# Optimization experiments

Measured on AMD Instinct MI355X. Metric: run time of the kernel, lower is better.

The kernel has to match this reference:

```python
import jax, jax.numpy as jnp
import numpy as np
import math

B, S, D, H = 4, 2048, 2048, 16
HD = D // H  # 128


def _alibi_slopes(n_heads):
    # standard ALiBi slopes: 2^(-8/n * (h+1))
    return jnp.asarray([2.0 ** (-8.0 / n_heads * (h + 1)) for h in range(n_heads)], dtype=jnp.float32)


def setup_inputs() -> dict:
    key = jax.random.key(0)
    ks = jax.random.split(key, 10)
    w = lambda k: jax.random.normal(k, (D, D), dtype=jnp.float32) * 0.02
    b = lambda k: jax.random.normal(k, (D,), dtype=jnp.float32) * 0.01
    return {
        "hidden_states": jax.random.normal(ks[0], (B, S, D), dtype=jnp.float32),
        "Wq": w(ks[1]), "bq": b(ks[2]),
        "Wk": w(ks[3]), "bk": b(ks[4]),
        "Wv": w(ks[5]), "bv": b(ks[6]),
        "Wo": w(ks[7]), "bo": b(ks[8]),
        "alibi_slopes": _alibi_slopes(H),
    }


def reference(hidden_states, Wq, bq, Wk, bk, Wv, bv, Wo, bo, alibi_slopes):
    Bn, t, _ = hidden_states.shape
    split = lambda x: x.reshape(Bn, t, H, HD).transpose(0, 2, 1, 3)  # [B,H,S,hd]
    q = split(hidden_states @ Wq.T + bq)
    k = split(hidden_states @ Wk.T + bk)
    v = split(hidden_states @ Wv.T + bv)

    scores = jnp.einsum("bhsd,bhtd->bhst", q, k)  # [B,H,S,S]
    pos = jnp.arange(t)
    # alibi bias added BEFORE the 1/sqrt(hd) scaling, as in the torch code
    rel = (pos[None, :] - pos[:, None]).astype(scores.dtype)  # j - i
    bias = alibi_slopes[:, None, None] * rel  # [H,S,S]
    scores = (scores + bias[None]) / math.sqrt(HD)
    # grok-style tanh rescaling
    scores = 30.0 * jnp.tanh(scores / 30.0)
    causal = pos[:, None] >= pos[None, :]  # [S,S]
    scores = jnp.where(causal[None, None], scores, -jnp.inf)
    probs = jax.nn.softmax(scores, axis=-1)
    ctx = jnp.einsum("bhst,bhtd->bhsd", probs, v)
    ctx = ctx.transpose(0, 2, 1, 3).reshape(Bn, t, D)
    return ctx @ Wo.T + bo
```

## Files before the change

kernel.cpp:

```cpp
#include <hip/hip_runtime.h>

typedef unsigned int u32;
typedef unsigned short u16;
typedef __bf16 bf16x8 __attribute__((ext_vector_type(8)));
typedef float f32x4 __attribute__((ext_vector_type(4)));


__device__ __forceinline__ u16 f2bf(float f) {
  u32 u = __builtin_bit_cast(u32, f);
  u32 r = u + 0x7fffu + ((u >> 16) & 1u);
  return (u16)(r >> 16);
}

__device__ __forceinline__ void gload_lds16(const void* g, void* l) {
  __builtin_amdgcn_global_load_lds(
      (__attribute__((address_space(1))) void*)(g),
      (__attribute__((address_space(3))) void*)(l), 16, 0, 0);
}


__global__ __launch_bounds__(256) void convert_kernel(
    const float* __restrict__ hs, const float* __restrict__ wq,
    const float* __restrict__ wk, const float* __restrict__ wv,
    const float* __restrict__ wo,
    u16* __restrict__ hsb, u16* __restrict__ wqb, u16* __restrict__ wkb,
    u16* __restrict__ wvb, u16* __restrict__ wob) {
  long t = (long)blockIdx.x * 256 + threadIdx.x;
  const float* src;
  u16* dst;
  long off;
  if (t < 2097152) {
    src = hs; dst = hsb; off = t << 3;
  } else {
    long u = t - 2097152;
    int wi = (int)(u >> 19);
    off = (u & 524287) << 3;
    if (wi == 0)      { src = wq; dst = wqb; }
    else if (wi == 1) { src = wk; dst = wkb; }
    else if (wi == 2) { src = wv; dst = wvb; }
    else              { src = wo; dst = wob; }
  }
  float4 a = *(const float4*)(src + off);
  float4 b = *(const float4*)(src + off + 4);
  uint4 o;
  o.x = (u32)f2bf(a.x) | ((u32)f2bf(a.y) << 16);
  o.y = (u32)f2bf(a.z) | ((u32)f2bf(a.w) << 16);
  o.z = (u32)f2bf(b.x) | ((u32)f2bf(b.y) << 16);
  o.w = (u32)f2bf(b.z) | ((u32)f2bf(b.w) << 16);
  *(uint4*)(dst + off) = o;
}


template <int OF32>
__global__ __launch_bounds__(512, 2) void gemm256_kernel(
    const u16* __restrict__ A, const u16* __restrict__ Bw,
    const float* __restrict__ bias0, const float* __restrict__ bias1,
    const float* __restrict__ bias2, void* __restrict__ o0,
    void* __restrict__ o1, void* __restrict__ o2, int m_tiles, int n_tiles) {
  __shared__ __align__(16) char L[2][2][2][16384];

  const int tid = threadIdx.x;
  const int lane = tid & 63, w = tid >> 6;
  const int lr = lane & 15, lk = lane >> 4;
  const int wm = (w >> 2) * 128, wn = (w & 3) * 64;

  const int bid = blockIdx.x;
  const int xcd = bid & 7, loc = bid >> 3;
  const int n_idx = xcd * (n_tiles >> 3) + loc / m_tiles;
  const int m_idx = loc % m_tiles;
  const int m0 = m_idx * 256, n0 = n_idx * 256;

  const char* Ab = (const char*)A;
  const char* Bb = (const char*)Bw;

  auto stage = [&](int t, int kh, int isB) {
    const char* G = isB ? Bb : Ab;
    const int r0 = isB ? n0 : m0;
    char* Ld = &L[t & 1][isB][kh][0];
    const size_t kb = (size_t)(t * 64 + kh * 32) * 2;
#pragma unroll
    for (int j = 0; j < 2; j++) {
      const int o = j * 8192 + tid * 16;
      const int row = o >> 6;
      const int c = (o & 63) ^ (((row >> 1) & 3) << 4);
      gload_lds16(G + (size_t)(r0 + row) * 4096 + kb + c, Ld + o);
    }
  };
  auto rdA = [&](bf16x8* dst, int buf, int kh, int mset) {
#pragma unroll
    for (int m = 0; m < 4; m++) {
      const int row = wm + mset * 64 + m * 16 + lr;
      const int c = (lk * 16) ^ (((row >> 1) & 3) << 4);
      dst[m] = *(const bf16x8*)(&L[buf][0][kh][0] + row * 64 + c);
    }
  };
  auto rdB = [&](bf16x8* dst, int buf, int kh) {
#pragma unroll
    for (int n = 0; n < 4; n++) {
      const int row = wn + n * 16 + lr;
      const int c = (lk * 16) ^ (((row >> 1) & 3) << 4);
      dst[n] = *(const bf16x8*)(&L[buf][1][kh][0] + row * 64 + c);
    }
  };

  f32x4 acc[2][4][4];
#pragma unroll
  for (int s = 0; s < 2; s++)
#pragma unroll
    for (int m = 0; m < 4; m++)
#pragma unroll
      for (int n = 0; n < 4; n++) acc[s][m][n] = {0.f, 0.f, 0.f, 0.f};

  auto mm = [&](f32x4 (&ac)[4][4], bf16x8* a_, bf16x8* b_) {
    __builtin_amdgcn_s_setprio(1);
#pragma unroll
    for (int m = 0; m < 4; m++)
#pragma unroll
      for (int n = 0; n < 4; n++)
        ac[m][n] = __builtin_amdgcn_mfma_f32_16x16x32_bf16(a_[m], b_[n],
                                                           ac[m][n], 0, 0, 0);
    __builtin_amdgcn_s_setprio(0);
  };

  stage(0, 0, 0); stage(0, 0, 1); stage(0, 1, 0); stage(0, 1, 1);
  stage(1, 0, 0); stage(1, 0, 1);
  asm volatile("s_waitcnt vmcnt(4)" ::: "memory");
  asm volatile("s_barrier" ::: "memory");

  bf16x8 af[4], af2[4], bf[4];
  for (int t = 0; t < 32; ++t) {
    const int buf = t & 1;
    const int t1 = (t + 1 < 32) ? t + 1 : 31;
    const int t2 = (t + 2 < 32) ? t + 2 : 31;
    stage(t1, 1, 0);
    rdA(af, buf, 0, 0); rdB(bf, buf, 0);
    asm volatile("s_barrier" ::: "memory");
    mm(acc[0], af, bf);
    asm volatile("s_barrier" ::: "memory");
    stage(t1, 1, 1);
    rdA(af2, buf, 0, 1);
    asm volatile("s_barrier" ::: "memory");
    mm(acc[1], af2, bf);
    asm volatile("s_barrier" ::: "memory");
    stage(t2, 0, 0);
    rdA(af, buf, 1, 0); rdB(bf, buf, 1);
    asm volatile("s_barrier" ::: "memory");
    mm(acc[0], af, bf);
    asm volatile("s_barrier" ::: "memory");
    stage(t2, 0, 1);
    rdA(af2, buf, 1, 1);
    asm volatile("s_barrier" ::: "memory");
    mm(acc[1], af2, bf);
    asm volatile("s_waitcnt vmcnt(4)" ::: "memory");
    asm volatile("s_barrier" ::: "memory");
  }
  asm volatile("s_waitcnt vmcnt(0)" ::: "memory");

  const float* bias;
  void* op;
  int nl0;
  if (OF32) {
    bias = bias0; op = o0; nl0 = n0;
  } else {
    const int seg = n0 >> 11;
    bias = seg == 0 ? bias0 : (seg == 1 ? bias1 : bias2);
    op = seg == 0 ? o0 : (seg == 1 ? o1 : o2);
    nl0 = n0 & 2047;
  }
#pragma unroll
  for (int n = 0; n < 4; n++) {
    const int col = nl0 + wn + n * 16 + lr;
    const float bv = bias[col];
#pragma unroll
    for (int s = 0; s < 2; s++)
#pragma unroll
      for (int m = 0; m < 4; m++) {
        const int grow = m0 + wm + s * 64 + m * 16 + lk * 4;
#pragma unroll
        for (int r = 0; r < 4; r++) {
          const float v = acc[s][m][n][r] + bv;
          if (OF32)
            ((float*)op)[(size_t)(grow + r) * 2048 + col] = v;
          else
            ((u16*)op)[(size_t)(grow + r) * 2048 + col] = f2bf(v);
        }
      }
  }
}


__global__ __launch_bounds__(512, 2) void attn_kernel(
    const u16* __restrict__ Qm, const u16* __restrict__ Km,
    const u16* __restrict__ Vm, const float* __restrict__ slopes,
    u16* __restrict__ ctx) {
  __shared__ __align__(16) char Ks[64 * 256];
  __shared__ __align__(16) char Vt[2][128 * 128];
  __shared__ __align__(16) char Pb[8][16 * 128];

  const int bid = blockIdx.x;
  const int sw = (bid & 7) * 64 + (bid >> 3);
  const int bh = sw >> 3, pi = sw & 7;
  const int b = bh >> 4, h = bh & 15;
  const int NTA = 2 * pi + 2;

  const int tid = threadIdx.x;
  const int lane = tid & 63, w = tid >> 6;
  const int lr = lane & 15, lk = lane >> 4;

  const char* Qb = (const char*)Qm + (size_t)b * 2048 * 4096 + h * 256;
  const char* Kb = (const char*)Km + (size_t)b * 2048 * 4096 + h * 256;
  const char* Vb = (const char*)Vm + (size_t)b * 2048 * 4096 + h * 256;

  const float SCALE = 0.08838834764831845f;
  const float sl_c = slopes[h] * SCALE;

  const float A0 = 1363.3468136400704f, A2 = 0.16831442143704573f,
              A4 = 1.7811049887518067e-6f;
  const float D0 = 945.0f, D2 = 0.4666666666666667f, D4 = 1.851851851851852e-5f;
  const float SH = -43.2808512266689f;

  float Tt[16];
#pragma unroll
  for (int nb = 0; nb < 4; nb++)
#pragma unroll
    for (int r = 0; r < 4; r++) Tt[nb * 4 + r] = sl_c * (float)(nb * 16 - r);

  const int vd0 = (tid & 15) * 8;
  const int vkv2 = tid >> 4;

  uint4 vr0, vr1;

  auto kvt_of = [&](int it) { return it < NTA ? it : it - NTA; };

  auto stageK = [&](int it) {
    const int kv0 = kvt_of(it) * 64;
#pragma unroll
    for (int j = 0; j < 2; j++) {
      const int o = j * 8192 + tid * 16;
      const int row = o >> 8, c = (o & 255) ^ ((row & 7) << 4);
      gload_lds16(Kb + (size_t)(kv0 + row) * 4096 + c, Ks + o);
    }
  };
  auto loadV = [&](int it) {
    const int kv0 = kvt_of(it) * 64;
    vr0 = *(const uint4*)(Vb + (size_t)(kv0 + vkv2 * 2) * 4096 + vd0 * 2);
    vr1 = *(const uint4*)(Vb + (size_t)(kv0 + vkv2 * 2 + 1) * 4096 + vd0 * 2);
  };
  auto writeV = [&](int bufi) {
    const u32* p0 = (const u32*)&vr0;
    const u32* p1 = (const u32*)&vr1;
#pragma unroll
    for (int wd = 0; wd < 4; wd++) {
      const u32 ev = __builtin_amdgcn_perm(p1[wd], p0[wd], 0x05040100u);
      const u32 od = __builtin_amdgcn_perm(p1[wd], p0[wd], 0x07060302u);
      const int d0_ = vd0 + 2 * wd, d1_ = d0_ + 1;
      *(u32*)(Vt[bufi] + d0_ * 128 +
              ((vkv2 * 4) ^ (((d0_ ^ (d0_ >> 3)) & 7) << 4))) = ev;
      *(u32*)(Vt[bufi] + d1_ * 128 +
              ((vkv2 * 4) ^ (((d1_ ^ (d1_ >> 3)) & 7) << 4))) = od;
    }
  };

  bf16x8 qf[4];
  f32x4 pv[8];
  float rs[4];
  int q0 = 0;

  stageK(0);
  loadV(0);

  for (int it = 0; it < 34; ++it) {
    const int bufi = it & 1;
    const int kv0 = kvt_of(it) * 64;

    if (it == 0 || it == NTA) {
      const int st = (it == 0) ? pi : (15 - pi);
      q0 = st * 128 + w * 16;
#pragma unroll
      for (int kc = 0; kc < 4; kc++)
        qf[kc] =
            *(const bf16x8*)(Qb + (size_t)(q0 + lr) * 4096 + kc * 64 + lk * 16);
#pragma unroll
      for (int i = 0; i < 8; i++) pv[i] = {0.f, 0.f, 0.f, 0.f};
      rs[0] = rs[1] = rs[2] = rs[3] = 0.f;
    }

    writeV(bufi);
    asm volatile("s_waitcnt vmcnt(0)" ::: "memory");
    __syncthreads();

    if (it + 1 < 34) loadV(it + 1);

    f32x4 sc[4];
    __builtin_amdgcn_s_setprio(1);
#pragma unroll
    for (int nb = 0; nb < 4; nb++) {
      f32x4 a = {0.f, 0.f, 0.f, 0.f};
      const int krow = nb * 16 + lr;
#pragma unroll
      for (int kc = 0; kc < 4; kc++) {
        const int off = krow * 256 + ((kc * 64 + lk * 16) ^ ((krow & 7) << 4));
        bf16x8 kf = *(const bf16x8*)(Ks + off);
        a = __builtin_amdgcn_mfma_f32_16x16x32_bf16(qf[kc], kf, a, 0, 0, 0);
      }
      sc[nb] = a;
    }
    __builtin_amdgcn_s_setprio(0);

    __syncthreads();
    if (it + 1 < 34) stageK(it + 1);

    const float aliB = sl_c * (float)(kv0 + lr - q0 - lk * 4);
#pragma unroll
    for (int nb = 0; nb < 4; nb++) {
      const int kv = kv0 + nb * 16 + lr;
#pragma unroll
      for (int r = 0; r < 4; r++) {
        const int q = q0 + lk * 4 + r;
        const float z = fmaf(sc[nb][r], SCALE, aliB + Tt[nb * 4 + r]);
        const float u = z * z;
        const float num = fmaf(u, fmaf(u, A4, A2), A0);
        const float den = fmaf(u, fmaf(u, D4, D2), D0);
        const float pa = fmaf(z * num, __builtin_amdgcn_rcpf(den), SH);
        float p = exp2f(pa);
        p = (kv <= q) ? p : 0.0f;
        rs[r] += p;
        const int qq = lk * 4 + r;
        const int off =
            qq * 128 + (((nb * 16 + lr) * 2) ^ ((qq & 12) << 3));
        const u32 ub = __builtin_bit_cast(u32, p);
        *(u16*)(Pb[w] + off) = (u16)((ub + 0x8000u) >> 16);
      }
    }

    __builtin_amdgcn_s_setprio(1);
#pragma unroll
    for (int kc = 0; kc < 2; kc++) {
      const int poff = lr * 128 + ((kc * 64 + lk * 16) ^ ((lr & 12) << 3));
      bf16x8 pf = *(const bf16x8*)(Pb[w] + poff);
#pragma unroll
      for (int db = 0; db < 8; db++) {
        const int d = db * 16 + lr;
        const int voff =
            d * 128 + ((kc * 64 + lk * 16) ^ (((d ^ (d >> 3)) & 7) << 4));
        bf16x8 vf = *(const bf16x8*)(Vt[bufi] + voff);
        pv[db] = __builtin_amdgcn_mfma_f32_16x16x32_bf16(pf, vf, pv[db], 0, 0, 0);
      }
    }
    __builtin_amdgcn_s_setprio(0);

    if (it == NTA - 1 || it == 33) {
      float inv[4];
#pragma unroll
      for (int r = 0; r < 4; r++) {
        float s = rs[r];
        s += __shfl_xor(s, 1);
        s += __shfl_xor(s, 2);
        s += __shfl_xor(s, 4);
        s += __shfl_xor(s, 8);
        inv[r] = 1.0f / s;
      }
      const size_t baserow = (size_t)b * 2048 + q0 + lk * 4;
#pragma unroll
      for (int db = 0; db < 8; db++)
#pragma unroll
        for (int r = 0; r < 4; r++)
          ctx[(baserow + r) * 2048 + h * 128 + db * 16 + lr] =
              f2bf(pv[db][r] * inv[r]);
    }
  }
}


extern "C" void kernel_launch(void* const* d_in, const int* in_sizes, int n_in,
                              void* d_out, int out_size, void* d_ws,
                              size_t ws_size, hipStream_t stream) {
  const float* hs = (const float*)d_in[0];
  const float* Wq = (const float*)d_in[1];
  const float* bq = (const float*)d_in[2];
  const float* Wk = (const float*)d_in[3];
  const float* bk = (const float*)d_in[4];
  const float* Wv = (const float*)d_in[5];
  const float* bv = (const float*)d_in[6];
  const float* Wo = (const float*)d_in[7];
  const float* bo = (const float*)d_in[8];
  const float* slopes = (const float*)d_in[9];

  char* ws = (char*)d_ws;
  u16* hsb = (u16*)(ws);
  u16* wqb = (u16*)(ws + 33554432);
  u16* wkb = (u16*)(ws + 41943040);
  u16* wvb = (u16*)(ws + 50331648);
  u16* wob = (u16*)(ws + 58720256);
  u16* Qb  = (u16*)(ws + 67108864);
  u16* Kb  = (u16*)(ws + 100663296);
  u16* Vb  = (u16*)(ws + 134217728);
  u16* ctxb = hsb;

  convert_kernel<<<16384, 256, 0, stream>>>(hs, Wq, Wk, Wv, Wo, hsb, wqb, wkb,
                                            wvb, wob);
  gemm256_kernel<0><<<768, 512, 0, stream>>>(hsb, wqb, bq, bk, bv, Qb, Kb, Vb,
                                             32, 24);
  attn_kernel<<<512, 512, 0, stream>>>(Qb, Kb, Vb, slopes, ctxb);
  gemm256_kernel<1><<<256, 512, 0, stream>>>(ctxb, wob, bo, bo, bo, d_out,
                                             d_out, d_out, 32, 8);
}
```

Measured before the change: 504.0 us.

## Restructure GEMM main loop into a software pipeline with fewer barriers

Rewrites the bf16 projection GEMM K-loop so register fragments for the second M half are carried across iterations. MFMAs now overlap with the next LDS reads and the global-to-LDS staging of the next tile. Barriers drop from eight per iteration to two, gated by vmcnt waits. Per-thread global base addresses are precomputed once, so staging only adds a K offset. The looser synchronisation leans on waitcnt ordering between waves, and on the last iteration it re-stages the same tile into a buffer that may still be being read.

Result: no change. 509.5 us (+1.1%).

```diff
diff --git a/kernel.cpp b/kernel.cpp
--- a/kernel.cpp
+++ b/kernel.cpp
@@ -72,19 +72,23 @@
 
   const char* Ab = (const char*)A;
   const char* Bb = (const char*)Bw;
+  const char* gA[2];
+  const char* gB[2];
+#pragma unroll
+  for (int j = 0; j < 2; j++) {
+    const int o = j * 8192 + tid * 16;
+    const int row = o >> 6;
+    const int c = (o & 63) ^ (((row >> 1) & 3) << 4);
+    gA[j] = Ab + (size_t)(m0 + row) * 4096 + c;
+    gB[j] = Bb + (size_t)(n0 + row) * 4096 + c;
+  }
 
   auto stage = [&](int t, int kh, int isB) {
-    const char* G = isB ? Bb : Ab;
-    const int r0 = isB ? n0 : m0;
-    char* Ld = &L[t & 1][isB][kh][0];
-    const size_t kb = (size_t)(t * 64 + kh * 32) * 2;
-#pragma unroll
-    for (int j = 0; j < 2; j++) {
-      const int o = j * 8192 + tid * 16;
-      const int row = o >> 6;
-      const int c = (o & 63) ^ (((row >> 1) & 3) << 4);
-      gload_lds16(G + (size_t)(r0 + row) * 4096 + kb + c, Ld + o);
-    }
+    char* Ld = &L[t & 1][isB][kh][0] + tid * 16;
+    const int gof = t * 128 + kh * 64;
+#pragma unroll
+    for (int j = 0; j < 2; j++)
+      gload_lds16((isB ? gB[j] : gA[j]) + gof, Ld + j * 8192);
   };
   auto rdA = [&](bf16x8* dst, int buf, int kh, int mset) {
 #pragma unroll
@@ -123,38 +127,31 @@
   };
 
   stage(0, 0, 0); stage(0, 0, 1); stage(0, 1, 0); stage(0, 1, 1);
-  stage(1, 0, 0); stage(1, 0, 1);
-  asm volatile("s_waitcnt vmcnt(4)" ::: "memory");
-  asm volatile("s_barrier" ::: "memory");
-
-  bf16x8 af[4], af2[4], bf[4];
+
+  bf16x8 aP[4], aQ[4], b0[4], b1[4];
   for (int t = 0; t < 32; ++t) {
     const int buf = t & 1;
     const int t1 = (t + 1 < 32) ? t + 1 : 31;
-    const int t2 = (t + 2 < 32) ? t + 2 : 31;
-    stage(t1, 1, 0);
-    rdA(af, buf, 0, 0); rdB(bf, buf, 0);
-    asm volatile("s_barrier" ::: "memory");
-    mm(acc[0], af, bf);
-    asm volatile("s_barrier" ::: "memory");
-    stage(t1, 1, 1);
-    rdA(af2, buf, 0, 1);
-    asm volatile("s_barrier" ::: "memory");
-    mm(acc[1], af2, bf);
-    asm volatile("s_barrier" ::: "memory");
-    stage(t2, 0, 0);
-    rdA(af, buf, 1, 0); rdB(bf, buf, 1);
-    asm volatile("s_barrier" ::: "memory");
-    mm(acc[0], af, bf);
-    asm volatile("s_barrier" ::: "memory");
-    stage(t2, 0, 1);
-    rdA(af2, buf, 1, 1);
-    asm volatile("s_barrier" ::: "memory");
-    mm(acc[1], af2, bf);
     asm volatile("s_waitcnt vmcnt(4)" ::: "memory");
     asm volatile("s_barrier" ::: "memory");
-  }
-  asm volatile("s_waitcnt vmcnt(0)" ::: "memory");
+    rdA(aP, buf, 0, 0);
+    rdB(b0, buf, 0);
+    stage(t1, 0, 0);
+    if (t) mm(acc[1], aQ, b1);
+    rdA(aQ, buf, 0, 1);
+    stage(t1, 0, 1);
+    mm(acc[0], aP, b0);
+    asm volatile("s_waitcnt vmcnt(4)" ::: "memory");
+    asm volatile("s_barrier" ::: "memory");
+    rdA(aP, buf, 1, 0);
+    rdB(b1, buf, 1);
+    stage(t1, 1, 0);
+    mm(acc[1], aQ, b0);
+    rdA(aQ, buf, 1, 1);
+    stage(t1, 1, 1);
+    mm(acc[0], aP, b1);
+  }
+  mm(acc[1], aQ, b1);
 
   const float* bias;
   void* op;
```
